# Kernel optimization log

Hardware: AMD Instinct MI355X
Metric: run time of the kernel (lower is better)

The kernel has to match this reference:

```python
import jax, jax.numpy as jnp
import numpy as np

N_ITERS = 3
EPS = 1e-5


def _ln(x, g, b):
    mu = jnp.mean(x, axis=-1, keepdims=True)
    var = jnp.mean((x - mu) ** 2, axis=-1, keepdims=True)
    return (x - mu) * jax.lax.rsqrt(var + EPS) * g + b


def setup_inputs() -> dict:
    key = jax.random.key(0)
    ks = iter(jax.random.split(key, 32))
    B, N, D_in, H, K = 128, 1024, 192, 128, 3

    def lin(o, i):
        w = (jax.random.normal(next(ks), (o, i)) / np.sqrt(i)).astype(jnp.float32)
        return w, jnp.zeros((o,), jnp.float32)

    Wp, bp = lin(H, D_in)
    Wq, bq = lin(H, H)
    Wk, bk = lin(H, H)
    Wv, bv = lin(H, H)
    Wih, bih = lin(3 * H, H)   # GRUCell input weights, stacked [r, z, n]
    Whh, bhh = lin(3 * H, H)   # GRUCell hidden weights
    W1, b1 = lin(2 * H, H)     # MLP expand
    W2, b2 = lin(H, 2 * H)     # MLP project
    ones = jnp.ones((H,), jnp.float32)
    zeros = jnp.zeros((H,), jnp.float32)

    return {
        "patch_tokens": jax.random.normal(next(ks), (B, N, D_in), jnp.float32),
        "noise": jax.random.normal(next(ks), (B, K, H), jnp.float32),
        "slot_mu": (jax.random.normal(next(ks), (1, K, H)) * 0.02).astype(jnp.float32),
        "slot_log_sigma": jnp.zeros((1, K, H), jnp.float32),
        "Wp": Wp, "bp": bp, "g_in": ones, "b_in": zeros,
        "Wq": Wq, "bq": bq, "Wk": Wk, "bk": bk, "Wv": Wv, "bv": bv,
        "Wih": Wih, "bih": bih, "Whh": Whh, "bhh": bhh,
        "g_s": ones, "b_s": zeros,
        "W1": W1, "b1": b1, "W2": W2, "b2": b2,
        "g_m": ones, "b_m": zeros,
    }


def reference(patch_tokens, noise, slot_mu, slot_log_sigma,
              Wp, bp, g_in, b_in,
              Wq, bq, Wk, bk, Wv, bv,
              Wih, bih, Whh, bhh,
              g_s, b_s, W1, b1, W2, b2, g_m, b_m):
    H = slot_mu.shape[-1]
    scale = 1.0 / jnp.sqrt(jnp.asarray(H, patch_tokens.dtype))

    # project + LayerNorm inputs once (k, v depend only on inputs -> hoisted)
    inputs = _ln(patch_tokens @ Wp.T + bp, g_in, b_in)      # (B, N, H)
    k = inputs @ Wk.T + bk                                  # (B, N, H)
    v = inputs @ Wv.T + bv                                  # (B, N, H)

    slots = slot_mu + jnp.exp(slot_log_sigma) * noise       # (B, K, H)

    def gru_cell(x, h):
        gi = x @ Wih.T + bih                                # (B, K, 3H)
        gh = h @ Whh.T + bhh
        ir, iz, inn = jnp.split(gi, 3, axis=-1)
        hr, hz, hn = jnp.split(gh, 3, axis=-1)
        r = jax.nn.sigmoid(ir + hr)
        z = jax.nn.sigmoid(iz + hz)
        n = jnp.tanh(inn + r * hn)
        return (1.0 - z) * n + z * h

    attn_weights = None
    for _ in range(N_ITERS):
        slots_prev = slots
        s = _ln(slots, g_s, b_s)
        q = s @ Wq.T + bq                                   # (B, K, H)
        attn = jnp.einsum('bkd,bnd->bkn', q, k) * scale     # (B, K, N)
        attn_weights = jax.nn.softmax(attn, axis=1)         # softmax over slots
        updates = jnp.einsum('bkn,bnd->bkd', attn_weights, v)
        slots = gru_cell(updates, slots_prev)
        h = _ln(slots, g_m, b_m)
        slots = slots + (jax.nn.gelu(h @ W1.T + b1, approximate=False) @ W2.T + b2)

    return slots, attn_weights
```

## Files before the change

### kernel.cpp

```cpp
#include <hip/hip_runtime.h>
#include <math.h>

constexpr float EPS = 1e-5f;
constexpr float SCALE = 0.08838834764831845f;

using f32x4  = __attribute__((ext_vector_type(4))) float;
using bf16x8 = __attribute__((ext_vector_type(8))) short;
using us8    = __attribute__((ext_vector_type(8))) unsigned short;

__device__ __forceinline__ unsigned short f2b_rne(float f) {
    unsigned int x = __float_as_uint(f);
    return (unsigned short)((x + 0x7fffu + ((x >> 16) & 1u)) >> 16);
}

__device__ __forceinline__ int swz32(int row, int k8) {
    int f = (row & 3) ^ ((row >> 2) & 3);
    return row * 32 + ((k8 ^ f) << 3);
}

__global__ __launch_bounds__(256) void prep_weights_kernel(
    const float* __restrict__ Wp, const float* __restrict__ Wk,
    const float* __restrict__ Wv, const float* __restrict__ Wih,
    const float* __restrict__ Whh, const float* __restrict__ W1,
    const float* __restrict__ W2, const float* __restrict__ Wq,
    unsigned short* __restrict__ hi, unsigned short* __restrict__ lo,
    float4* __restrict__ wt4)
{
    int idx = blockIdx.x * 256 + threadIdx.x;
    if (idx < 57344) {
        float v;
        if (idx < 24576)      v = Wp[idx];
        else if (idx < 40960) v = Wk[idx - 24576];
        else                  v = Wv[idx - 40960];
        unsigned int bits = __float_as_uint(v);
        hi[idx] = (unsigned short)(bits >> 16);
        lo[idx] = f2b_rne(v - __uint_as_float(bits & 0xffff0000u));
    } else {
        int li = idx - 57344;
        const float* src; int OUT, base, K;
        if (li < 12288)      { src = Wih; OUT = 384; base = 0;     K = 128; }
        else if (li < 24576) { src = Whh; OUT = 384; base = 12288; K = 128; }
        else if (li < 32768) { src = W1;  OUT = 256; base = 24576; K = 128; }
        else if (li < 40960) { src = W2;  OUT = 128; base = 32768; K = 256; }
        else                 { src = Wq;  OUT = 128; base = 40960; K = 128; }
        int lo2 = li - base;
        int kq = lo2 / OUT, t = lo2 - kq * OUT;
        float4 v;
        v.x = src[(size_t)t * K + 4 * kq];
        v.y = src[(size_t)t * K + 4 * kq + 1];
        v.z = src[(size_t)t * K + 4 * kq + 2];
        v.w = src[(size_t)t * K + 4 * kq + 3];
        wt4[li] = v;
    }
}

__global__ __launch_bounds__(256, 3) void fused_proj_kv_kernel(
    const float* __restrict__ patch,
    const unsigned short* __restrict__ Wphi, const unsigned short* __restrict__ Wplo,
    const unsigned short* __restrict__ Wkhi, const unsigned short* __restrict__ Wklo,
    const unsigned short* __restrict__ Wvhi, const unsigned short* __restrict__ Wvlo,
    const float* __restrict__ biasp, const float* __restrict__ g_in,
    const float* __restrict__ b_in, const float* __restrict__ biask,
    const float* __restrict__ biasv,
    float* __restrict__ kout, float* __restrict__ vout)
{
    __shared__ __align__(16) unsigned short mem[24576];

    const int tid  = threadIdx.x;
    const int lane = tid & 63, wave = tid >> 6;
    const int ln15 = lane & 15, quad = lane >> 4;
    const int bid  = blockIdx.x;
    const int m0   = ((bid & 7) * 256 + (bid >> 3)) * 64;

    const int wrow = wave * 16;
    f32x4 acc1[8];
#pragma unroll
    for (int nt = 0; nt < 8; nt++)
#pragma unroll
        for (int r = 0; r < 4; r++) acc1[nt][r] = 0.f;

    const int arow = tid >> 2, ak8 = tid & 3;
    const float* aptr = patch + (size_t)(m0 + arow) * 192 + ak8 * 8;
    float4 pa[6][2];
#pragma unroll
    for (int t6 = 0; t6 < 6; t6++) {
        pa[t6][0] = *(const float4*)(aptr + t6 * 32);
        pa[t6][1] = *(const float4*)(aptr + t6 * 32 + 4);
    }
    us8 pbh[2], pbl[2];
    int boff[2];
#pragma unroll
    for (int i = 0; i < 2; i++) {
        int c = tid + 256 * i;
        boff[i] = (c >> 2) * 192 + (c & 3) * 8;
        pbh[i] = *(const us8*)(Wphi + boff[i]);
        pbl[i] = *(const us8*)(Wplo + boff[i]);
    }

    const int ea = swz32(wrow + ln15, quad);

#pragma unroll
    for (int st = 0; st < 6; st++) {
        {
            float va[8] = {pa[st][0].x, pa[st][0].y, pa[st][0].z, pa[st][0].w,
                           pa[st][1].x, pa[st][1].y, pa[st][1].z, pa[st][1].w};
            us8 h, l;
#pragma unroll
            for (int j = 0; j < 8; j++) {
                unsigned int bits = __float_as_uint(va[j]);
                h[j] = (unsigned short)(bits >> 16);
                l[j] = f2b_rne(va[j] - __uint_as_float(bits & 0xffff0000u));
            }
            int e = swz32(arow, ak8);
            *(us8*)&mem[e]        = h;
            *(us8*)&mem[2048 + e] = l;
        }
#pragma unroll
        for (int i = 0; i < 2; i++) {
            int c = tid + 256 * i;
            int e = swz32(c >> 2, c & 3);
            *(us8*)&mem[4096 + e] = pbh[i];
            *(us8*)&mem[8192 + e] = pbl[i];
        }
        __syncthreads();

        if (st < 5) {
            int kn = (st + 1) * 32;
#pragma unroll
            for (int i = 0; i < 2; i++) {
                pbh[i] = *(const us8*)(Wphi + boff[i] + kn);
                pbl[i] = *(const us8*)(Wplo + boff[i] + kn);
            }
        }

        bf16x8 ah = *(const bf16x8*)&mem[ea];
        bf16x8 al = *(const bf16x8*)&mem[2048 + ea];
#pragma unroll
        for (int nt = 0; nt < 8; nt++) {
            int eb = swz32(nt * 16 + ln15, quad);
            bf16x8 bh = *(const bf16x8*)&mem[4096 + eb];
            bf16x8 bl = *(const bf16x8*)&mem[8192 + eb];
            acc1[nt] = __builtin_amdgcn_mfma_f32_16x16x32_bf16(ah, bh, acc1[nt], 0, 0, 0);
            acc1[nt] = __builtin_amdgcn_mfma_f32_16x16x32_bf16(ah, bl, acc1[nt], 0, 0, 0);
            acc1[nt] = __builtin_amdgcn_mfma_f32_16x16x32_bf16(al, bh, acc1[nt], 0, 0, 0);
        }
        __syncthreads();
    }

    us8 pw[4];
#pragma unroll
    for (int i = 0; i < 4; i++) {
        const unsigned short* pl = (i >> 1) ? Wklo : Wkhi;
        int c = tid + (i & 1) * 256;
        pw[i] = *(const us8*)(pl + (size_t)(c >> 2) * 128 + (c & 3) * 8);
    }

    {
        float bb[8], gg[8], be[8];
#pragma unroll
        for (int nt = 0; nt < 8; nt++) {
            int col = nt * 16 + ln15;
            bb[nt] = biasp[col]; gg[nt] = g_in[col]; be[nt] = b_in[col];
        }
#pragma unroll
        for (int nt = 0; nt < 8; nt++)
#pragma unroll
            for (int r = 0; r < 4; r++) acc1[nt][r] += bb[nt];

        float mu[4], rs[4];
#pragma unroll
        for (int r = 0; r < 4; r++) {
            float s = 0.f, s2 = 0.f;
#pragma unroll
            for (int nt = 0; nt < 8; nt++) {
                float v = acc1[nt][r];
                s += v; s2 += v * v;
            }
#pragma unroll
            for (int off = 1; off < 16; off <<= 1) {
                s  += __shfl_xor(s,  off, 64);
                s2 += __shfl_xor(s2, off, 64);
            }
            float m = s * (1.f / 128.f);
            mu[r] = m;
            rs[r] = rsqrtf(s2 * (1.f / 128.f) - m * m + EPS);
        }
#pragma unroll
        for (int nt = 0; nt < 8; nt++)
#pragma unroll
            for (int r = 0; r < 4; r++) {
                float v = (acc1[nt][r] - mu[r]) * rs[r] * gg[nt] + be[nt];
                int row = wrow + quad * 4 + r, col = nt * 16 + ln15;
                int xi = (row * 128 + col) ^ ((row & 7) << 3);
                unsigned int bits = __float_as_uint(v);
                mem[xi]        = (unsigned short)(bits >> 16);
                mem[8192 + xi] = f2b_rne(v - __uint_as_float(bits & 0xffff0000u));
            }
    }

    const int R  = (wave & 1) * 32;
    const int Cb = (wave >> 1) * 64;
    const int xorx = (ln15 & 7) << 3;

    float bbk[4], bbv[4];
#pragma unroll
    for (int nt = 0; nt < 4; nt++) {
        int col = Cb + nt * 16 + ln15;
        bbk[nt] = biask[col];
        bbv[nt] = biasv[col];
    }

    f32x4 acc[2][4];
#pragma unroll
    for (int mt = 0; mt < 2; mt++)
#pragma unroll
        for (int nt = 0; nt < 4; nt++)
#pragma unroll
            for (int r = 0; r < 4; r++) acc[mt][nt][r] = 0.f;

#pragma unroll
    for (int s = 0; s < 8; s++) {
#pragma unroll
        for (int i = 0; i < 4; i++) {
            int c = tid + (i & 1) * 256;
            int e = 16384 + (i >> 1) * 4096 + swz32(c >> 2, c & 3);
            *(us8*)&mem[e] = pw[i];
        }
        __syncthreads();

        if (s < 7) {
            int sn = s + 1, kkn = (sn & 3) * 32;
            const unsigned short* ph = (sn >> 2) ? Wvhi : Wkhi;
            const unsigned short* po = (sn >> 2) ? Wvlo : Wklo;
#pragma unroll
            for (int i = 0; i < 4; i++) {
                const unsigned short* pl = (i >> 1) ? po : ph;
                int c = tid + (i & 1) * 256;
                pw[i] = *(const us8*)(pl + (size_t)(c >> 2) * 128 + (c & 3) * 8 + kkn);
            }
        }

        int kk = (s & 3) * 32;
        bf16x8 xh[2], xl[2];
#pragma unroll
        for (int mt = 0; mt < 2; mt++) {
            int row = R + mt * 16 + ln15;
            int ei = (row * 128 + kk + quad * 8) ^ xorx;
            xh[mt] = *(const bf16x8*)&mem[ei];
            xl[mt] = *(const bf16x8*)&mem[8192 + ei];
        }
#pragma unroll
        for (int nt = 0; nt < 4; nt++) {
            int eb = 16384 + swz32(Cb + nt * 16 + ln15, quad);
            bf16x8 wh = *(const bf16x8*)&mem[eb];
            bf16x8 wl = *(const bf16x8*)&mem[4096 + eb];
#pragma unroll
            for (int mt = 0; mt < 2; mt++) {
                acc[mt][nt] = __builtin_amdgcn_mfma_f32_16x16x32_bf16(xh[mt], wh, acc[mt][nt], 0, 0, 0);
                acc[mt][nt] = __builtin_amdgcn_mfma_f32_16x16x32_bf16(xh[mt], wl, acc[mt][nt], 0, 0, 0);
                acc[mt][nt] = __builtin_amdgcn_mfma_f32_16x16x32_bf16(xl[mt], wh, acc[mt][nt], 0, 0, 0);
            }
        }

        if (s == 3) {
#pragma unroll
            for (int mt = 0; mt < 2; mt++)
#pragma unroll
                for (int nt = 0; nt < 4; nt++)
#pragma unroll
                    for (int r = 0; r < 4; r++) {
                        size_t o = (size_t)(m0 + R + mt * 16 + quad * 4 + r) * 128
                                 + Cb + nt * 16 + ln15;
                        kout[o] = acc[mt][nt][r] + bbk[nt];
                        acc[mt][nt][r] = 0.f;
                    }
        }
        if (s < 7) __syncthreads();
    }

#pragma unroll
    for (int mt = 0; mt < 2; mt++)
#pragma unroll
        for (int nt = 0; nt < 4; nt++)
#pragma unroll
            for (int r = 0; r < 4; r++) {
                size_t o = (size_t)(m0 + R + mt * 16 + quad * 4 + r) * 128
                         + Cb + nt * 16 + ln15;
                vout[o] = acc[mt][nt][r] + bbv[nt];
            }
}

__global__ __launch_bounds__(128) void init_lnq_kernel(
    const float* __restrict__ noise, const float* __restrict__ smu,
    const float* __restrict__ sls, const float* __restrict__ g_s,
    const float* __restrict__ b_s, const float4* __restrict__ WqT4,
    const float* __restrict__ bq, float* __restrict__ slots,
    float* __restrict__ q)
{
    __shared__ float s_l[128];
    __shared__ float red[4];
    const int row = blockIdx.x, tid = threadIdx.x;
    const int k = row % 3;
    float x = smu[k * 128 + tid] + expf(sls[k * 128 + tid]) * noise[row * 128 + tid];
    slots[row * 128 + tid] = x;

    float s = x, s2 = x * x;
#pragma unroll
    for (int off = 32; off >= 1; off >>= 1) {
        s += __shfl_down(s, off, 64); s2 += __shfl_down(s2, off, 64);
    }
    if ((tid & 63) == 0) { red[tid >> 6] = s; red[2 + (tid >> 6)] = s2; }
    __syncthreads();
    float S = red[0] + red[1], S2 = red[2] + red[3];
    float m = S * (1.f / 128.f);
    float r = rsqrtf(S2 * (1.f / 128.f) - m * m + EPS);
    s_l[tid] = (x - m) * r * g_s[tid] + b_s[tid];
    __syncthreads();

    float a = bq[tid];
#pragma unroll 8
    for (int kq = 0; kq < 32; kq++) {
        float4 w = WqT4[kq * 128 + tid];
        a += s_l[4 * kq] * w.x + s_l[4 * kq + 1] * w.y
           + s_l[4 * kq + 2] * w.z + s_l[4 * kq + 3] * w.w;
    }
    q[row * 128 + tid] = a;
}

__global__ __launch_bounds__(256) void attn_kernel(
    const float* __restrict__ q, const float* __restrict__ kbuf,
    const float* __restrict__ vbuf, float* __restrict__ upd_part,
    float* __restrict__ attn_out, int write_attn)
{
    __shared__ float q_l[3][132];
    __shared__ float lg[3][256];
    __shared__ float w_l[3][256];
    __shared__ float part[8][3][128];
    const int b = blockIdx.y, chunk = blockIdx.x, n0 = chunk * 256, tid = threadIdx.x;

    for (int idx = tid; idx < 384; idx += 256) {
        int s = idx >> 7, c = idx & 127;
        q_l[s][c + (c >> 5)] = q[b * 384 + idx];
    }

    const int n = tid >> 2, q4 = tid & 3;
    const float4* kg4 = (const float4*)(kbuf + ((size_t)b * 1024 + n0 + n) * 128 + q4 * 32);
    const int tg = tid >> 5, d0 = (tid & 31) * 4;
    const float* vp = vbuf + ((size_t)b * 1024 + n0 + tg * 8) * 128 + d0;

    float4 ka[8], kb2[8], va[8], vb2[8];
#pragma unroll
    for (int i = 0; i < 8; i++) ka[i] = kg4[i];
    __syncthreads();

    const float* q0 = &q_l[0][q4 * 33];
    const float* q1 = &q_l[1][q4 * 33];
    const float* q2 = &q_l[2][q4 * 33];
#pragma unroll
    for (int sc = 0; sc < 4; sc++) {
        if (sc < 3) {
            const float4* kn = kg4 + (size_t)(sc + 1) * 2048;
#pragma unroll
            for (int i = 0; i < 8; i++) ((sc & 1) ? ka : kb2)[i] = kn[i];
        } else {
#pragma unroll
            for (int j = 0; j < 8; j++) va[j] = *(const float4*)(vp + (size_t)j * 128);
        }
        const float4* kc = (sc & 1) ? kb2 : ka;
        float p0 = 0.f, p1 = 0.f, p2 = 0.f;
#pragma unroll
        for (int i = 0; i < 8; i++) {
            float kx[4] = {kc[i].x, kc[i].y, kc[i].z, kc[i].w};
#pragma unroll
            for (int j = 0; j < 4; j++) {
                float vv = kx[j];
                p0 += q0[4 * i + j] * vv;
                p1 += q1[4 * i + j] * vv;
                p2 += q2[4 * i + j] * vv;
            }
        }
        p0 += __shfl_xor(p0, 1, 64); p0 += __shfl_xor(p0, 2, 64);
        p1 += __shfl_xor(p1, 1, 64); p1 += __shfl_xor(p1, 2, 64);
        p2 += __shfl_xor(p2, 1, 64); p2 += __shfl_xor(p2, 2, 64);
        if (q4 == 0) {
            lg[0][sc * 64 + n] = p0 * SCALE;
            lg[1][sc * 64 + n] = p1 * SCALE;
            lg[2][sc * 64 + n] = p2 * SCALE;
        }
    }
    __syncthreads();

    {
        float l0 = lg[0][tid], l1 = lg[1][tid], l2 = lg[2][tid];
        float m = fmaxf(l0, fmaxf(l1, l2));
        float e0 = expf(l0 - m), e1 = expf(l1 - m), e2 = expf(l2 - m);
        float inv = 1.f / (e0 + e1 + e2);
        w_l[0][tid] = e0 * inv; w_l[1][tid] = e1 * inv; w_l[2][tid] = e2 * inv;
        if (write_attn) {
            int nn = n0 + tid;
            attn_out[b * 3072 + nn]        = e0 * inv;
            attn_out[b * 3072 + 1024 + nn] = e1 * inv;
            attn_out[b * 3072 + 2048 + nn] = e2 * inv;
        }
    }
    __syncthreads();

    float4 a0 = {0.f, 0.f, 0.f, 0.f}, a1 = a0, a2 = a0;
#pragma unroll
    for (int sc = 0; sc < 4; sc++) {
        if (sc < 3) {
            const float* vn = vp + (size_t)(sc + 1) * 8192;
#pragma unroll
            for (int j = 0; j < 8; j++)
                ((sc & 1) ? va : vb2)[j] = *(const float4*)(vn + (size_t)j * 128);
        }
        const float4* vc = (sc & 1) ? vb2 : va;
#pragma unroll
        for (int j = 0; j < 8; j++) {
            float w0 = w_l[0][sc * 64 + tg * 8 + j];
            float w1 = w_l[1][sc * 64 + tg * 8 + j];
            float w2 = w_l[2][sc * 64 + tg * 8 + j];
            float4 vv = vc[j];
            a0.x += w0 * vv.x; a0.y += w0 * vv.y; a0.z += w0 * vv.z; a0.w += w0 * vv.w;
            a1.x += w1 * vv.x; a1.y += w1 * vv.y; a1.z += w1 * vv.z; a1.w += w1 * vv.w;
            a2.x += w2 * vv.x; a2.y += w2 * vv.y; a2.z += w2 * vv.z; a2.w += w2 * vv.w;
        }
    }
    *(float4*)&part[tg][0][d0] = a0;
    *(float4*)&part[tg][1][d0] = a1;
    *(float4*)&part[tg][2][d0] = a2;
    __syncthreads();

    for (int idx = tid; idx < 384; idx += 256) {
        int s = idx >> 7, d = idx & 127;
        float u = 0.f;
#pragma unroll
        for (int g = 0; g < 8; g++) u += part[g][s][d];
        upd_part[(((size_t)b * 4 + chunk) * 3 + s) * 128 + d] = u;
    }
}

__global__ __launch_bounds__(384) void gru_mlp_kernel(
    const float* __restrict__ slots_in, const float* __restrict__ upd_part,
    const float4* __restrict__ WihT4, const float* __restrict__ bih,
    const float4* __restrict__ WhhT4, const float* __restrict__ bhh,
    const float* __restrict__ g_m, const float* __restrict__ b_m,
    const float4* __restrict__ W1T4, const float* __restrict__ b1,
    const float4* __restrict__ W2T4, const float* __restrict__ b2,
    const float* __restrict__ g_s, const float* __restrict__ b_s,
    const float4* __restrict__ WqT4, const float* __restrict__ bq,
    float* __restrict__ slots_out, float* __restrict__ q_out, int write_q)
{
    __shared__ float u2[2][128];
    __shared__ float u_l[128], h_l[128];
    __shared__ float r_l[128], z_l[128], in_l[128], hn_l[128];
    __shared__ float n_l[128], hid_l[256], w2p[256];
    __shared__ float red[4];
    const int row = blockIdx.x, tid = threadIdx.x;
    const int bb_ = row / 3, ss = row - bb_ * 3;

    if (tid < 256) {
        int col = tid & 127, half = tid >> 7;
        const float* up = upd_part + (((size_t)bb_ * 4 + half * 2) * 3 + ss) * 128 + col;
        float u = 0.f;
#pragma unroll
        for (int c = 0; c < 2; c++) u += up[(size_t)c * 384];
        u2[half][col] = u;
        if (half == 0) h_l[col] = slots_in[row * 128 + col];
    }
    __syncthreads();
    if (tid < 128) u_l[tid] = u2[0][tid] + u2[1][tid];
    __syncthreads();

    {
        float gi = bih[tid], gh = bhh[tid];
#pragma unroll 8
        for (int kq = 0; kq < 32; kq++) {
            float4 a = WihT4[kq * 384 + tid];
            float4 c = WhhT4[kq * 384 + tid];
            gi += u_l[4 * kq] * a.x + u_l[4 * kq + 1] * a.y
                + u_l[4 * kq + 2] * a.z + u_l[4 * kq + 3] * a.w;
            gh += h_l[4 * kq] * c.x + h_l[4 * kq + 1] * c.y
                + h_l[4 * kq + 2] * c.z + h_l[4 * kq + 3] * c.w;
        }
        if (tid < 128)      r_l[tid] = 1.f / (1.f + expf(-(gi + gh)));
        else if (tid < 256) z_l[tid - 128] = 1.f / (1.f + expf(-(gi + gh)));
        else { in_l[tid - 256] = gi; hn_l[tid - 256] = gh; }
    }
    __syncthreads();

    float hnew = 0.f;
    if (tid < 128) {
        float nn = tanhf(in_l[tid] + r_l[tid] * hn_l[tid]);
        hnew = (1.f - z_l[tid]) * nn + z_l[tid] * h_l[tid];
        float s = hnew, s2 = hnew * hnew;
#pragma unroll
        for (int off = 32; off >= 1; off >>= 1) {
            s += __shfl_down(s, off, 64); s2 += __shfl_down(s2, off, 64);
        }
        if ((tid & 63) == 0) { red[tid >> 6] = s; red[2 + (tid >> 6)] = s2; }
    }
    __syncthreads();
    if (tid < 128) {
        float S = red[0] + red[1], S2 = red[2] + red[3];
        float m1 = S * (1.f / 128.f);
        float r1 = rsqrtf(S2 * (1.f / 128.f) - m1 * m1 + EPS);
        n_l[tid] = (hnew - m1) * r1 * g_m[tid] + b_m[tid];
    }
    __syncthreads();

    if (tid < 256) {
        float a = b1[tid];
#pragma unroll 8
        for (int kq = 0; kq < 32; kq++) {
            float4 w = W1T4[kq * 256 + tid];
            a += n_l[4 * kq] * w.x + n_l[4 * kq + 1] * w.y
               + n_l[4 * kq + 2] * w.z + n_l[4 * kq + 3] * w.w;
        }
        a = 0.5f * a * (1.f + erff(a * 0.70710678118654752f));
        hid_l[tid] = a;
    }
    __syncthreads();

    if (tid < 256) {
        int out = tid & 127, half = tid >> 7;
        float p = 0.f;
#pragma unroll 8
        for (int kq = half * 32; kq < half * 32 + 32; kq++) {
            float4 w = W2T4[kq * 128 + out];
            p += hid_l[4 * kq] * w.x + hid_l[4 * kq + 1] * w.y
               + hid_l[4 * kq + 2] * w.z + hid_l[4 * kq + 3] * w.w;
        }
        w2p[tid] = p;
    }
    __syncthreads();

    float snew = 0.f;
    if (tid < 128) {
        snew = hnew + b2[tid] + (w2p[tid] + w2p[128 + tid]);
        slots_out[row * 128 + tid] = snew;
    }

    if (write_q) {
        if (tid < 128) {
            float t1 = snew, t2 = snew * snew;
#pragma unroll
            for (int off = 32; off >= 1; off >>= 1) {
                t1 += __shfl_down(t1, off, 64); t2 += __shfl_down(t2, off, 64);
            }
            if ((tid & 63) == 0) { red[tid >> 6] = t1; red[2 + (tid >> 6)] = t2; }
        }
        __syncthreads();
        if (tid < 128) {
            float T = red[0] + red[1], T2 = red[2] + red[3];
            float m2 = T * (1.f / 128.f);
            float r2 = rsqrtf(T2 * (1.f / 128.f) - m2 * m2 + EPS);
            n_l[tid] = (snew - m2) * r2 * g_s[tid] + b_s[tid];
        }
        __syncthreads();
        if (tid < 256) {
            int out = tid & 127, half = tid >> 7;
            float p = (half == 0) ? bq[out] : 0.f;
#pragma unroll 8
            for (int kq = half * 16; kq < half * 16 + 16; kq++) {
                float4 w = WqT4[kq * 128 + out];
                p += n_l[4 * kq] * w.x + n_l[4 * kq + 1] * w.y
                   + n_l[4 * kq + 2] * w.z + n_l[4 * kq + 3] * w.w;
            }
            w2p[tid] = p;
        }
        __syncthreads();
        if (tid < 128) q_out[row * 128 + tid] = w2p[tid] + w2p[128 + tid];
    }
}

extern "C" void kernel_launch(void* const* d_in, const int* in_sizes, int n_in,
                              void* d_out, int out_size, void* d_ws, size_t ws_size,
                              hipStream_t stream)
{
    const float* patch   = (const float*)d_in[0];
    const float* noise   = (const float*)d_in[1];
    const float* slot_mu = (const float*)d_in[2];
    const float* slot_ls = (const float*)d_in[3];
    const float* Wp = (const float*)d_in[4];  const float* bp = (const float*)d_in[5];
    const float* g_in = (const float*)d_in[6]; const float* b_in = (const float*)d_in[7];
    const float* Wq = (const float*)d_in[8];  const float* bq = (const float*)d_in[9];
    const float* Wk = (const float*)d_in[10]; const float* bk = (const float*)d_in[11];
    const float* Wv = (const float*)d_in[12]; const float* bv = (const float*)d_in[13];
    const float* Wih = (const float*)d_in[14]; const float* bih = (const float*)d_in[15];
    const float* Whh = (const float*)d_in[16]; const float* bhh = (const float*)d_in[17];
    const float* g_s = (const float*)d_in[18]; const float* b_s = (const float*)d_in[19];
    const float* W1 = (const float*)d_in[20]; const float* b1 = (const float*)d_in[21];
    const float* W2 = (const float*)d_in[22]; const float* b2 = (const float*)d_in[23];
    const float* g_m = (const float*)d_in[24]; const float* b_m = (const float*)d_in[25];

    float* kbuf = (float*)d_ws;
    float* vbuf = kbuf + 16777216;
    unsigned short* w_hi = (unsigned short*)(vbuf + 16777216);
    unsigned short* w_lo = w_hi + 57344;
    unsigned short* wp_hi = w_hi,        * wp_lo = w_lo;
    unsigned short* wk_hi = w_hi + 24576,* wk_lo = w_lo + 24576;
    unsigned short* wv_hi = w_hi + 40960,* wv_lo = w_lo + 40960;
    float4* wt4 = (float4*)(w_lo + 57344);
    float4* wihT4 = wt4;
    float4* whhT4 = wt4 + 12288;
    float4* w1T4  = wt4 + 24576;
    float4* w2T4  = wt4 + 32768;
    float4* wqT4  = wt4 + 40960;
    float* slots = (float*)(wt4 + 45056);
    float* qbuf  = slots + 49152;
    float* part  = qbuf + 49152;

    float* out_slots = (float*)d_out;
    float* out_attn  = (float*)d_out + 49152;

    prep_weights_kernel<<<400, 256, 0, stream>>>(
        Wp, Wk, Wv, Wih, Whh, W1, W2, Wq, w_hi, w_lo, wt4);

    fused_proj_kv_kernel<<<2048, 256, 0, stream>>>(
        patch, wp_hi, wp_lo, wk_hi, wk_lo, wv_hi, wv_lo,
        bp, g_in, b_in, bk, bv, kbuf, vbuf);

    init_lnq_kernel<<<384, 128, 0, stream>>>(noise, slot_mu, slot_ls,
                                             g_s, b_s, wqT4, bq, slots, qbuf);

    for (int it = 0; it < 3; it++) {
        attn_kernel<<<dim3(4, 128), 256, 0, stream>>>(
            qbuf, kbuf, vbuf, part, out_attn, it == 2 ? 1 : 0);
        gru_mlp_kernel<<<384, 384, 0, stream>>>(
            slots, part, wihT4, bih, whhT4, bhh, g_m, b_m, w1T4, b1, w2T4, b2,
            g_s, b_s, wqT4, bq,
            (it == 2) ? out_slots : slots, qbuf, it == 2 ? 0 : 1);
    }
}
```

Measured before the change: 358.9 us.

## Fold Wk into query and Wv after attention, storing only normalized inputs

Stops materializing K and V and stores only the layer-normed projected inputs, packed as hi/lo bf16 in a 32-bit word. Wk is folded into the query (q·Wk plus a q·bk bias term), and Wv is applied to the attention-weighted input sum inside the GRU kernel, with bv scaled by the sum of the attention weights. This drops two large GEMMs and cuts the workspace written and read by the attention passes from two fp32 tensors to one. The cost is extra small matvecs per slot, weight-sum reductions, and a slightly different rounding path.

```diff
diff --git a/kernel.cpp b/kernel.cpp
--- a/kernel.cpp
+++ b/kernel.cpp
@@ -11,6 +11,9 @@
 __device__ __forceinline__ unsigned short f2b_rne(float f) {
     unsigned int x = __float_as_uint(f);
     return (unsigned short)((x + 0x7fffu + ((x >> 16) & 1u)) >> 16);
+}
+__device__ __forceinline__ float xrec(unsigned int w) {
+    return __uint_as_float(w & 0xffff0000u) + __uint_as_float(w << 16);
 }
 
 __device__ __forceinline__ int swz32(int row, int k8) {
@@ -27,44 +30,47 @@
     float4* __restrict__ wt4)
 {
     int idx = blockIdx.x * 256 + threadIdx.x;
-    if (idx < 57344) {
-        float v;
-        if (idx < 24576)      v = Wp[idx];
-        else if (idx < 40960) v = Wk[idx - 24576];
-        else                  v = Wv[idx - 40960];
+    if (idx < 24576) {
+        float v = Wp[idx];
         unsigned int bits = __float_as_uint(v);
         hi[idx] = (unsigned short)(bits >> 16);
         lo[idx] = f2b_rne(v - __uint_as_float(bits & 0xffff0000u));
     } else {
-        int li = idx - 57344;
-        const float* src; int OUT, base, K;
-        if (li < 12288)      { src = Wih; OUT = 384; base = 0;     K = 128; }
-        else if (li < 24576) { src = Whh; OUT = 384; base = 12288; K = 128; }
-        else if (li < 32768) { src = W1;  OUT = 256; base = 24576; K = 128; }
-        else if (li < 40960) { src = W2;  OUT = 128; base = 32768; K = 256; }
-        else                 { src = Wq;  OUT = 128; base = 40960; K = 128; }
-        int lo2 = li - base;
-        int kq = lo2 / OUT, t = lo2 - kq * OUT;
+        int li = idx - 24576;
         float4 v;
-        v.x = src[(size_t)t * K + 4 * kq];
-        v.y = src[(size_t)t * K + 4 * kq + 1];
-        v.z = src[(size_t)t * K + 4 * kq + 2];
-        v.w = src[(size_t)t * K + 4 * kq + 3];
+        if (li < 49152) {
+            const float* src; int OUT, base, K;
+            if (li < 12288)      { src = Wih; OUT = 384; base = 0;     K = 128; }
+            else if (li < 24576) { src = Whh; OUT = 384; base = 12288; K = 128; }
+            else if (li < 32768) { src = W1;  OUT = 256; base = 24576; K = 128; }
+            else if (li < 40960) { src = W2;  OUT = 128; base = 32768; K = 256; }
+            else if (li < 45056) { src = Wq;  OUT = 128; base = 40960; K = 128; }
+            else                 { src = Wv;  OUT = 128; base = 45056; K = 128; }
+            int l2 = li - base;
+            int kq = l2 / OUT, t = l2 - kq * OUT;
+            v.x = src[(size_t)t * K + 4 * kq];
+            v.y = src[(size_t)t * K + 4 * kq + 1];
+            v.z = src[(size_t)t * K + 4 * kq + 2];
+            v.w = src[(size_t)t * K + 4 * kq + 3];
+        } else {
+            int l2 = li - 49152;
+            int kq = l2 >> 7, t = l2 & 127;
+            v.x = Wk[(size_t)(4 * kq + 0) * 128 + t];
+            v.y = Wk[(size_t)(4 * kq + 1) * 128 + t];
+            v.z = Wk[(size_t)(4 * kq + 2) * 128 + t];
+            v.w = Wk[(size_t)(4 * kq + 3) * 128 + t];
+        }
         wt4[li] = v;
     }
 }
 
-__global__ __launch_bounds__(256, 3) void fused_proj_kv_kernel(
+__global__ __launch_bounds__(256, 4) void fused_proj_x_kernel(
     const float* __restrict__ patch,
     const unsigned short* __restrict__ Wphi, const unsigned short* __restrict__ Wplo,
-    const unsigned short* __restrict__ Wkhi, const unsigned short* __restrict__ Wklo,
-    const unsigned short* __restrict__ Wvhi, const unsigned short* __restrict__ Wvlo,
     const float* __restrict__ biasp, const float* __restrict__ g_in,
-    const float* __restrict__ b_in, const float* __restrict__ biask,
-    const float* __restrict__ biasv,
-    float* __restrict__ kout, float* __restrict__ vout)
+    const float* __restrict__ b_in, unsigned int* __restrict__ xbuf)
 {
-    __shared__ __align__(16) unsigned short mem[24576];
+    __shared__ __align__(16) unsigned short mem[12288];
 
     const int tid  = threadIdx.x;
     const int lane = tid & 63, wave = tid >> 6;
@@ -147,155 +153,55 @@
         __syncthreads();
     }
 
-    us8 pw[4];
-#pragma unroll
-    for (int i = 0; i < 4; i++) {
-        const unsigned short* pl = (i >> 1) ? Wklo : Wkhi;
-        int c = tid + (i & 1) * 256;
-        pw[i] = *(const us8*)(pl + (size_t)(c >> 2) * 128 + (c & 3) * 8);
-    }
-
-    {
-        float bb[8], gg[8], be[8];
+    float bb[8], gg[8], be[8];
+#pragma unroll
+    for (int nt = 0; nt < 8; nt++) {
+        int col = nt * 16 + ln15;
+        bb[nt] = biasp[col]; gg[nt] = g_in[col]; be[nt] = b_in[col];
+    }
+#pragma unroll
+    for (int nt = 0; nt < 8; nt++)
+#pragma unroll
+        for (int r = 0; r < 4; r++) acc1[nt][r] += bb[nt];
+
+    float mu[4], rs[4];
+#pragma unroll
+    for (int r = 0; r < 4; r++) {
+        float s = 0.f, s2 = 0.f;
 #pragma unroll
         for (int nt = 0; nt < 8; nt++) {
-            int col = nt * 16 + ln15;
-            bb[nt] = biasp[col]; gg[nt] = g_in[col]; be[nt] = b_in[col];
-        }
-#pragma unroll
-        for (int nt = 0; nt < 8; nt++)
-#pragma unroll
-            for (int r = 0; r < 4; r++) acc1[nt][r] += bb[nt];
-
-        float mu[4], rs[4];
+            float v = acc1[nt][r];
+            s += v; s2 += v * v;
+        }
+#pragma unroll
+        for (int off = 1; off < 16; off <<= 1) {
+            s  += __shfl_xor(s,  off, 64);
+            s2 += __shfl_xor(s2, off, 64);
+        }
+        float m = s * (1.f / 128.f);
+        mu[r] = m;
+        rs[r] = rsqrtf(s2 * (1.f / 128.f) - m * m + EPS);
+    }
+#pragma unroll
+    for (int nt = 0; nt < 8; nt++)
 #pragma unroll
         for (int r = 0; r < 4; r++) {
-            float s = 0.f, s2 = 0.f;
-#pragma unroll
-            for (int nt = 0; nt < 8; nt++) {
-                float v = acc1[nt][r];
-                s += v; s2 += v * v;
-            }
-#pragma unroll
-            for (int off = 1; off < 16; off <<= 1) {
-                s  += __shfl_xor(s,  off, 64);
-                s2 += __shfl_xor(s2, off, 64);
-            }
-            float m = s * (1.f / 128.f);
-            mu[r] = m;
-            rs[r] = rsqrtf(s2 * (1.f / 128.f) - m * m + EPS);
-        }
-#pragma unroll
-        for (int nt = 0; nt < 8; nt++)
-#pragma unroll
-            for (int r = 0; r < 4; r++) {
-                float v = (acc1[nt][r] - mu[r]) * rs[r] * gg[nt] + be[nt];
-                int row = wrow + quad * 4 + r, col = nt * 16 + ln15;
-                int xi = (row * 128 + col) ^ ((row & 7) << 3);
-                unsigned int bits = __float_as_uint(v);
-                mem[xi]        = (unsigned short)(bits >> 16);
-                mem[8192 + xi] = f2b_rne(v - __uint_as_float(bits & 0xffff0000u));
-            }
-    }
-
-    const int R  = (wave & 1) * 32;
-    const int Cb = (wave >> 1) * 64;
-    const int xorx = (ln15 & 7) << 3;
-
-    float bbk[4], bbv[4];
-#pragma unroll
-    for (int nt = 0; nt < 4; nt++) {
-        int col = Cb + nt * 16 + ln15;
-        bbk[nt] = biask[col];
-        bbv[nt] = biasv[col];
-    }
-
-    f32x4 acc[2][4];
-#pragma unroll
-    for (int mt = 0; mt < 2; mt++)
-#pragma unroll
-        for (int nt = 0; nt < 4; nt++)
-#pragma unroll
-            for (int r = 0; r < 4; r++) acc[mt][nt][r] = 0.f;
-
-#pragma unroll
-    for (int s = 0; s < 8; s++) {
-#pragma unroll
-        for (int i = 0; i < 4; i++) {
-            int c = tid + (i & 1) * 256;
-            int e = 16384 + (i >> 1) * 4096 + swz32(c >> 2, c & 3);
-            *(us8*)&mem[e] = pw[i];
-        }
-        __syncthreads();
-
-        if (s < 7) {
-            int sn = s + 1, kkn = (sn & 3) * 32;
-            const unsigned short* ph = (sn >> 2) ? Wvhi : Wkhi;
-            const unsigned short* po = (sn >> 2) ? Wvlo : Wklo;
-#pragma unroll
-            for (int i = 0; i < 4; i++) {
-                const unsigned short* pl = (i >> 1) ? po : ph;
-                int c = tid + (i & 1) * 256;
-                pw[i] = *(const us8*)(pl + (size_t)(c >> 2) * 128 + (c & 3) * 8 + kkn);
-            }
-        }
-
-        int kk = (s & 3) * 32;
-        bf16x8 xh[2], xl[2];
-#pragma unroll
-        for (int mt = 0; mt < 2; mt++) {
-            int row = R + mt * 16 + ln15;
-            int ei = (row * 128 + kk + quad * 8) ^ xorx;
-            xh[mt] = *(const bf16x8*)&mem[ei];
-            xl[mt] = *(const bf16x8*)&mem[8192 + ei];
-        }
-#pragma unroll
-        for (int nt = 0; nt < 4; nt++) {
-            int eb = 16384 + swz32(Cb + nt * 16 + ln15, quad);
-            bf16x8 wh = *(const bf16x8*)&mem[eb];
-            bf16x8 wl = *(const bf16x8*)&mem[4096 + eb];
-#pragma unroll
-            for (int mt = 0; mt < 2; mt++) {
-                acc[mt][nt] = __builtin_amdgcn_mfma_f32_16x16x32_bf16(xh[mt], wh, acc[mt][nt], 0, 0, 0);
-                acc[mt][nt] = __builtin_amdgcn_mfma_f32_16x16x32_bf16(xh[mt], wl, acc[mt][nt], 0, 0, 0);
-                acc[mt][nt] = __builtin_amdgcn_mfma_f32_16x16x32_bf16(xl[mt], wh, acc[mt][nt], 0, 0, 0);
-            }
-        }
-
-        if (s == 3) {
-#pragma unroll
-            for (int mt = 0; mt < 2; mt++)
-#pragma unroll
-                for (int nt = 0; nt < 4; nt++)
-#pragma unroll
-                    for (int r = 0; r < 4; r++) {
-                        size_t o = (size_t)(m0 + R + mt * 16 + quad * 4 + r) * 128
-                                 + Cb + nt * 16 + ln15;
-                        kout[o] = acc[mt][nt][r] + bbk[nt];
-                        acc[mt][nt][r] = 0.f;
-                    }
-        }
-        if (s < 7) __syncthreads();
-    }
-
-#pragma unroll
-    for (int mt = 0; mt < 2; mt++)
-#pragma unroll
-        for (int nt = 0; nt < 4; nt++)
-#pragma unroll
-            for (int r = 0; r < 4; r++) {
-                size_t o = (size_t)(m0 + R + mt * 16 + quad * 4 + r) * 128
-                         + Cb + nt * 16 + ln15;
-                vout[o] = acc[mt][nt][r] + bbv[nt];
-            }
+            float v = (acc1[nt][r] - mu[r]) * rs[r] * gg[nt] + be[nt];
+            unsigned int bits = __float_as_uint(v);
+            unsigned int hi = bits & 0xffff0000u;
+            unsigned int word = hi | (unsigned int)f2b_rne(v - __uint_as_float(hi));
+            size_t o = (size_t)(m0 + wrow + quad * 4 + r) * 128 + nt * 16 + ln15;
+            xbuf[o] = word;
+        }
 }
 
 __global__ __launch_bounds__(128) void init_lnq_kernel(
     const float* __restrict__ noise, const float* __restrict__ smu,
     const float* __restrict__ sls, const float* __restrict__ g_s,
     const float* __restrict__ b_s, const float4* __restrict__ WqT4,
-    const float* __restrict__ bq, float* __restrict__ slots,
-    float* __restrict__ q)
+    const float* __restrict__ bq, const float4* __restrict__ WkQ4,
+    const float* __restrict__ bk, float* __restrict__ slots,
+    float* __restrict__ qk_out, float* __restrict__ qb_out)
 {
     __shared__ float s_l[128];
     __shared__ float red[4];
@@ -324,68 +230,86 @@
         a += s_l[4 * kq] * w.x + s_l[4 * kq + 1] * w.y
            + s_l[4 * kq + 2] * w.z + s_l[4 * kq + 3] * w.w;
     }
-    q[row * 128 + tid] = a;
+    __syncthreads();
+    s_l[tid] = a;
+    float pb = a * bk[tid];
+#pragma unroll
+    for (int off = 32; off >= 1; off >>= 1) pb += __shfl_down(pb, off, 64);
+    if ((tid & 63) == 0) red[tid >> 6] = pb;
+    __syncthreads();
+
+    float qkv = 0.f;
+#pragma unroll 8
+    for (int kq = 0; kq < 32; kq++) {
+        float4 w = WkQ4[kq * 128 + tid];
+        qkv += s_l[4 * kq] * w.x + s_l[4 * kq + 1] * w.y
+             + s_l[4 * kq + 2] * w.z + s_l[4 * kq + 3] * w.w;
+    }
+    qk_out[row * 128 + tid] = qkv;
+    if (tid == 0) qb_out[row] = red[0] + red[1];
 }
 
 __global__ __launch_bounds__(256) void attn_kernel(
-    const float* __restrict__ q, const float* __restrict__ kbuf,
-    const float* __restrict__ vbuf, float* __restrict__ upd_part,
-    float* __restrict__ attn_out, int write_attn)
+    const float* __restrict__ qk, const float* __restrict__ qb,
+    const unsigned int* __restrict__ xbuf, float* __restrict__ uX_part,
+    float* __restrict__ wsum_part, float* __restrict__ attn_out, int write_attn)
 {
-    __shared__ float q_l[3][132];
+    __shared__ float qk_l[3][132];
     __shared__ float lg[3][256];
     __shared__ float w_l[3][256];
     __shared__ float part[8][3][128];
+    __shared__ float wred[3][4];
     const int b = blockIdx.y, chunk = blockIdx.x, n0 = chunk * 256, tid = threadIdx.x;
 
     for (int idx = tid; idx < 384; idx += 256) {
         int s = idx >> 7, c = idx & 127;
-        q_l[s][c + (c >> 5)] = q[b * 384 + idx];
-    }
+        qk_l[s][c + (c >> 5)] = qk[b * 384 + idx];
+    }
+    const float qb0 = qb[b * 3], qb1 = qb[b * 3 + 1], qb2 = qb[b * 3 + 2];
 
     const int n = tid >> 2, q4 = tid & 3;
-    const float4* kg4 = (const float4*)(kbuf + ((size_t)b * 1024 + n0 + n) * 128 + q4 * 32);
+    const uint4* xg = (const uint4*)(xbuf + ((size_t)b * 1024 + n0 + n) * 128 + q4 * 32);
     const int tg = tid >> 5, d0 = (tid & 31) * 4;
-    const float* vp = vbuf + ((size_t)b * 1024 + n0 + tg * 8) * 128 + d0;
-
-    float4 ka[8], kb2[8], va[8], vb2[8];
-#pragma unroll
-    for (int i = 0; i < 8; i++) ka[i] = kg4[i];
-    __syncthreads();
-
-    const float* q0 = &q_l[0][q4 * 33];
-    const float* q1 = &q_l[1][q4 * 33];
-    const float* q2 = &q_l[2][q4 * 33];
+    const unsigned int* xp = xbuf + ((size_t)b * 1024 + n0 + tg * 8) * 128 + d0;
+
+    uint4 ka[8], kb2_[8], va[8], vb2_[8];
+#pragma unroll
+    for (int i = 0; i < 8; i++) ka[i] = xg[i];
+    __syncthreads();
+
+    const float* q0 = &qk_l[0][q4 * 33];
+    const float* q1 = &qk_l[1][q4 * 33];
+    const float* q2 = &qk_l[2][q4 * 33];
 #pragma unroll
     for (int sc = 0; sc < 4; sc++) {
         if (sc < 3) {
-            const float4* kn = kg4 + (size_t)(sc + 1) * 2048;
-#pragma unroll
-            for (int i = 0; i < 8; i++) ((sc & 1) ? ka : kb2)[i] = kn[i];
+            const uint4* kn = xg + (size_t)(sc + 1) * 2048;
+#pragma unroll
+            for (int i = 0; i < 8; i++) ((sc & 1) ? ka : kb2_)[i] = kn[i];
         } else {
 #pragma unroll
-            for (int j = 0; j < 8; j++) va[j] = *(const float4*)(vp + (size_t)j * 128);
-        }
-        const float4* kc = (sc & 1) ? kb2 : ka;
+            for (int j = 0; j < 8; j++) va[j] = *(const uint4*)(xp + (size_t)j * 128);
+        }
+        const uint4* kc = (sc & 1) ? kb2_ : ka;
         float p0 = 0.f, p1 = 0.f, p2 = 0.f;
 #pragma unroll
         for (int i = 0; i < 8; i++) {
-            float kx[4] = {kc[i].x, kc[i].y, kc[i].z, kc[i].w};
+            unsigned int kw[4] = {kc[i].x, kc[i].y, kc[i].z, kc[i].w};
 #pragma unroll
             for (int j = 0; j < 4; j++) {
-                float vv = kx[j];
-                p0 += q0[4 * i + j] * vv;
-                p1 += q1[4 * i + j] * vv;
-                p2 += q2[4 * i + j] * vv;
+                float xv = xrec(kw[j]);
+                p0 += q0[4 * i + j] * xv;
+                p1 += q1[4 * i + j] * xv;
+                p2 += q2[4 * i + j] * xv;
             }
         }
         p0 += __shfl_xor(p0, 1, 64); p0 += __shfl_xor(p0, 2, 64);
         p1 += __shfl_xor(p1, 1, 64); p1 += __shfl_xor(p1, 2, 64);
         p2 += __shfl_xor(p2, 1, 64); p2 += __shfl_xor(p2, 2, 64);
         if (q4 == 0) {
-            lg[0][sc * 64 + n] = p0 * SCALE;
-            lg[1][sc * 64 + n] = p1 * SCALE;
-            lg[2][sc * 64 + n] = p2 * SCALE;
+            lg[0][sc * 64 + n] = (p0 + qb0) * SCALE;
+            lg[1][sc * 64 + n] = (p1 + qb1) * SCALE;
+            lg[2][sc * 64 + n] = (p2 + qb2) * SCALE;
         }
     }
     __syncthreads();
@@ -395,12 +319,24 @@
         float m = fmaxf(l0, fmaxf(l1, l2));
         float e0 = expf(l0 - m), e1 = expf(l1 - m), e2 = expf(l2 - m);
         float inv = 1.f / (e0 + e1 + e2);
-        w_l[0][tid] = e0 * inv; w_l[1][tid] = e1 * inv; w_l[2][tid] = e2 * inv;
+        float w0 = e0 * inv, w1 = e1 * inv, w2 = e2 * inv;
+        w_l[0][tid] = w0; w_l[1][tid] = w1; w_l[2][tid] = w2;
         if (write_attn) {
             int nn = n0 + tid;
-            attn_out[b * 3072 + nn]        = e0 * inv;
-            attn_out[b * 3072 + 1024 + nn] = e1 * inv;
-            attn_out[b * 3072 + 2048 + nn] = e2 * inv;
+            attn_out[b * 3072 + nn]        = w0;
+            attn_out[b * 3072 + 1024 + nn] = w1;
+            attn_out[b * 3072 + 2048 + nn] = w2;
+        }
+        float s0 = w0, s1 = w1, s2 = w2;
+#pragma unroll
+        for (int off = 1; off < 64; off <<= 1) {
+            s0 += __shfl_xor(s0, off, 64);
+            s1 += __shfl_xor(s1, off, 64);
+            s2 += __shfl_xor(s2, off, 64);
+        }
+        if ((tid & 63) == 0) {
+            int wv = tid >> 6;
+            wred[0][wv] = s0; wred[1][wv] = s1; wred[2][wv] = s2;
         }
     }
     __syncthreads();
@@ -409,21 +345,22 @@
 #pragma unroll
     for (int sc = 0; sc < 4; sc++) {
         if (sc < 3) {
-            const float* vn = vp + (size_t)(sc + 1) * 8192;
+            const unsigned int* vn = xp + (size_t)(sc + 1) * 8192;
 #pragma unroll
             for (int j = 0; j < 8; j++)
-                ((sc & 1) ? va : vb2)[j] = *(const float4*)(vn + (size_t)j * 128);
-        }
-        const float4* vc = (sc & 1) ? vb2 : va;
+                ((sc & 1) ? va : vb2_)[j] = *(const uint4*)(vn + (size_t)j * 128);
+        }
+        const uint4* vc = (sc & 1) ? vb2_ : va;
 #pragma unroll
         for (int j = 0; j < 8; j++) {
             float w0 = w_l[0][sc * 64 + tg * 8 + j];
             float w1 = w_l[1][sc * 64 + tg * 8 + j];
             float w2 = w_l[2][sc * 64 + tg * 8 + j];
-            float4 vv = vc[j];
-            a0.x += w0 * vv.x; a0.y += w0 * vv.y; a0.z += w0 * vv.z; a0.w += w0 * vv.w;
-            a1.x += w1 * vv.x; a1.y += w1 * vv.y; a1.z += w1 * vv.z; a1.w += w1 * vv.w;
-            a2.x += w2 * vv.x; a2.y += w2 * vv.y; a2.z += w2 * vv.z; a2.w += w2 * vv.w;
+            unsigned int vw[4] = {vc[j].x, vc[j].y, vc[j].z, vc[j].w};
+            float x0 = xrec(vw[0]), x1 = xrec(vw[1]), x2 = xrec(vw[2]), x3 = xrec(vw[3]);
+            a0.x += w0 * x0; a0.y += w0 * x1; a0.z += w0 * x2; a0.w += w0 * x3;
+            a1.x += w1 * x0; a1.y += w1 * x1; a1.z += w1 * x2; a1.w += w1 * x3;
+            a2.x += w2 * x0; a2.y += w2 * x1; a2.z += w2 * x2; a2.w += w2 * x3;
         }
     }
     *(float4*)&part[tg][0][d0] = a0;
@@ -436,12 +373,17 @@
         float u = 0.f;
 #pragma unroll
         for (int g = 0; g < 8; g++) u += part[g][s][d];
-        upd_part[(((size_t)b * 4 + chunk) * 3 + s) * 128 + d] = u;
-    }
+        uX_part[(((size_t)b * 4 + chunk) * 3 + s) * 128 + d] = u;
+    }
+    if (tid < 3)
+        wsum_part[((size_t)b * 4 + chunk) * 3 + tid] =
+            (wred[tid][0] + wred[tid][1]) + (wred[tid][2] + wred[tid][3]);
 }
 
 __global__ __launch_bounds__(384) void gru_mlp_kernel(
-    const float* __restrict__ slots_in, const float* __restrict__ upd_part,
+    const float* __restrict__ slots_in, const float* __restrict__ uX_part,
+    const float* __restrict__ wsum_part,
+    const float4* __restrict__ WvT4, const float* __restrict__ bv,
     const float4* __restrict__ WihT4, const float* __restrict__ bih,
     const float4* __restrict__ WhhT4, const float* __restrict__ bhh,
     const float* __restrict__ g_m, const float* __restrict__ b_m,
@@ -449,30 +391,48 @@
     const float4* __restrict__ W2T4, const float* __restrict__ b2,
     const float* __restrict__ g_s, const float* __restrict__ b_s,
     const float4* __restrict__ WqT4, const float* __restrict__ bq,
-    float* __restrict__ slots_out, float* __restrict__ q_out, int write_q)
+    const float4* __restrict__ WkQ4, const float* __restrict__ bk,
+    float* __restrict__ slots_out, float* __restrict__ qk_out,
+    float* __restrict__ qb_out, int write_q)
 {
     __shared__ float u2[2][128];
-    __shared__ float u_l[128], h_l[128];
+    __shared__ float uxs[128], u_l[128], h_l[128];
     __shared__ float r_l[128], z_l[128], in_l[128], hn_l[128];
     __shared__ float n_l[128], hid_l[256], w2p[256];
     __shared__ float red[4];
+    __shared__ float wsum_s;
     const int row = blockIdx.x, tid = threadIdx.x;
     const int bb_ = row / 3, ss = row - bb_ * 3;
 
     if (tid < 256) {
         int col = tid & 127, half = tid >> 7;
-        const float* up = upd_part + (((size_t)bb_ * 4 + half * 2) * 3 + ss) * 128 + col;
-        float u = 0.f;
-#pragma unroll
-        for (int c = 0; c < 2; c++) u += up[(size_t)c * 384];
-        u2[half][col] = u;
+        const float* up = uX_part + (((size_t)bb_ * 4 + half * 2) * 3 + ss) * 128 + col;
+        u2[half][col] = up[0] + up[384];
         if (half == 0) h_l[col] = slots_in[row * 128 + col];
-    }
-    __syncthreads();
-    if (tid < 128) u_l[tid] = u2[0][tid] + u2[1][tid];
-    __syncthreads();
-
-    {
+    } else if (tid == 256) {
+        const float* wp = wsum_part + (size_t)bb_ * 12 + ss;
+        wsum_s = ((wp[0] + wp[3]) + wp[6]) + wp[9];
+    }
+    __syncthreads();
+    if (tid < 128) uxs[tid] = u2[0][tid] + u2[1][tid];
+    __syncthreads();
+
+    if (tid < 256) {
+        int out = tid & 127, half = tid >> 7;
+        float p = 0.f;
+#pragma unroll 8
+        for (int kq = half * 16; kq < half * 16 + 16; kq++) {
+            float4 w = WvT4[kq * 128 + out];
+            p += uxs[4 * kq] * w.x + uxs[4 * kq + 1] * w.y
+               + uxs[4 * kq + 2] * w.z + uxs[4 * kq + 3] * w.w;
+        }
+        w2p[tid] = p;
+    }
+    __syncthreads();
+    if (tid < 128) u_l[tid] = (w2p[tid] + w2p[128 + tid]) + wsum_s * bv[tid];
+    __syncthreads();
+
+    if (tid < 384) {
         float gi = bih[tid], gh = bhh[tid];
 #pragma unroll 8
         for (int kq = 0; kq < 32; kq++) {
@@ -570,7 +530,29 @@
             w2p[tid] = p;
         }
         __syncthreads();
-        if (tid < 128) q_out[row * 128 + tid] = w2p[tid] + w2p[128 + tid];
+        if (tid < 128) {
+            float qv = w2p[tid] + w2p[128 + tid];
+            n_l[tid] = qv;
+            float pb = qv * bk[tid];
+#pragma unroll
+            for (int off = 32; off >= 1; off >>= 1) pb += __shfl_down(pb, off, 64);
+            if ((tid & 63) == 0) red[tid >> 6] = pb;
+        }
+        __syncthreads();
+        if (tid == 0) qb_out[row] = red[0] + red[1];
+        if (tid < 256) {
+            int out = tid & 127, half = tid >> 7;
+            float p = 0.f;
+#pragma unroll 8
+            for (int kq = half * 16; kq < half * 16 + 16; kq++) {
+                float4 w = WkQ4[kq * 128 + out];
+                p += n_l[4 * kq] * w.x + n_l[4 * kq + 1] * w.y
+                   + n_l[4 * kq + 2] * w.z + n_l[4 * kq + 3] * w.w;
+            }
+            hid_l[half * 128 + out] = p;
+        }
+        __syncthreads();
+        if (tid < 128) qk_out[row * 128 + tid] = hid_l[tid] + hid_l[128 + tid];
     }
 }
 
@@ -594,42 +576,42 @@
     const float* W2 = (const float*)d_in[22]; const float* b2 = (const float*)d_in[23];
     const float* g_m = (const float*)d_in[24]; const float* b_m = (const float*)d_in[25];
 
-    float* kbuf = (float*)d_ws;
-    float* vbuf = kbuf + 16777216;
-    unsigned short* w_hi = (unsigned short*)(vbuf + 16777216);
-    unsigned short* w_lo = w_hi + 57344;
-    unsigned short* wp_hi = w_hi,        * wp_lo = w_lo;
-    unsigned short* wk_hi = w_hi + 24576,* wk_lo = w_lo + 24576;
-    unsigned short* wv_hi = w_hi + 40960,* wv_lo = w_lo + 40960;
-    float4* wt4 = (float4*)(w_lo + 57344);
+    unsigned int* xbuf = (unsigned int*)d_ws;
+    unsigned short* wp_hi = (unsigned short*)(xbuf + 16777216);
+    unsigned short* wp_lo = wp_hi + 24576;
+    float4* wt4 = (float4*)(wp_lo + 24576);
     float4* wihT4 = wt4;
     float4* whhT4 = wt4 + 12288;
     float4* w1T4  = wt4 + 24576;
     float4* w2T4  = wt4 + 32768;
     float4* wqT4  = wt4 + 40960;
-    float* slots = (float*)(wt4 + 45056);
-    float* qbuf  = slots + 49152;
-    float* part  = qbuf + 49152;
+    float4* wvT4  = wt4 + 45056;
+    float4* wkQ4  = wt4 + 49152;
+    float* slots  = (float*)(wt4 + 53248);
+    float* qkbuf  = slots + 49152;
+    float* qbbuf  = qkbuf + 49152;
+    float* part   = qbbuf + 384;
+    float* wsum   = part + 196608;
 
     float* out_slots = (float*)d_out;
     float* out_attn  = (float*)d_out + 49152;
 
-    prep_weights_kernel<<<400, 256, 0, stream>>>(
-        Wp, Wk, Wv, Wih, Whh, W1, W2, Wq, w_hi, w_lo, wt4);
-
-    fused_proj_kv_kernel<<<2048, 256, 0, stream>>>(
-        patch, wp_hi, wp_lo, wk_hi, wk_lo, wv_hi, wv_lo,
-        bp, g_in, b_in, bk, bv, kbuf, vbuf);
+    prep_weights_kernel<<<304, 256, 0, stream>>>(
+        Wp, Wk, Wv, Wih, Whh, W1, W2, Wq, wp_hi, wp_lo, wt4);
+
+    fused_proj_x_kernel<<<2048, 256, 0, stream>>>(
+        patch, wp_hi, wp_lo, bp, g_in, b_in, xbuf);
 
     init_lnq_kernel<<<384, 128, 0, stream>>>(noise, slot_mu, slot_ls,
-                                             g_s, b_s, wqT4, bq, slots, qbuf);
+                                             g_s, b_s, wqT4, bq, wkQ4, bk,
+                                             slots, qkbuf, qbbuf);
 
     for (int it = 0; it < 3; it++) {
         attn_kernel<<<dim3(4, 128), 256, 0, stream>>>(
-            qbuf, kbuf, vbuf, part, out_attn, it == 2 ? 1 : 0);
+            qkbuf, qbbuf, xbuf, part, wsum, out_attn, it == 2 ? 1 : 0);
         gru_mlp_kernel<<<384, 384, 0, stream>>>(
-            slots, part, wihT4, bih, whhT4, bhh, g_m, b_m, w1T4, b1, w2T4, b2,
-            g_s, b_s, wqT4, bq,
-            (it == 2) ? out_slots : slots, qbuf, it == 2 ? 0 : 1);
-    }
-}
+            slots, part, wsum, wvT4, bv, wihT4, bih, whhT4, bhh, g_m, b_m,
+            w1T4, b1, w2T4, b2, g_s, b_s, wqT4, bq, wkQ4, bk,
+            (it == 2) ? out_slots : slots, qkbuf, qbbuf, it == 2 ? 0 : 1);
+    }
+}
```

Measured after the change: 351.7 us. 1.02x faster.
